# Kernel tuning notes

Measured on AMD Instinct MI355X. Metric: run time of the kernel, lower is better.

The kernel has to match this reference:

```python
import jax, jax.numpy as jnp
import numpy as np

H, W = 512, 512  # spatial shape from init_kwargs
N_PTS = 200000
C_IN, C_OUT, K, PAD = 64, 128, 3, 1


def setup_inputs() -> dict:
    key = jax.random.key(0)
    k1, k2, k3, k4 = jax.random.split(key, 4)
    batch_size = 4
    features = jax.random.normal(k1, (N_PTS, C_IN), dtype=jnp.float32)
    b = jax.random.randint(k2, (N_PTS, 1), 0, batch_size, dtype=jnp.int32)
    yx = jax.random.randint(k3, (N_PTS, 2), 0, H, dtype=jnp.int32)  # y,x in [0, 512)
    coors = jnp.concatenate([b, yx], axis=1)  # [N, 3] = (batch, y, x)
    # spconv conv weight, expressed OIHW for lax.conv
    weight = jax.random.normal(k4, (C_OUT, C_IN, K, K), dtype=jnp.float32) * (1.0 / np.sqrt(C_IN * K * K))
    return {"features": features, "coors": coors, "batch_size": batch_size, "weight": weight}


def reference(features, coors, batch_size, weight):
    # SparseConvTensor -> densify: scatter-add point features onto the [B, C, H, W] grid
    # (add is faithful to spconv's gather-GEMM-scatter handling of duplicate coords).
    dense = jnp.zeros((batch_size, features.shape[1], H, W), dtype=features.dtype)
    dense = dense.at[coors[:, 0], :, coors[:, 1], coors[:, 2]].add(features)
    # SparseConv2d(stride=1, padding=1, bias=None) == dense conv on the densified grid;
    # inactive output sites are exactly zero, so this matches the densified sparse output.
    out = jax.lax.conv_general_dilated(
        dense, weight,
        window_strides=(1, 1),
        padding=[(PAD, PAD), (PAD, PAD)],
        dimension_numbers=("NCHW", "OIHW", "NCHW"),
    )
    return out  # [B, C_out, H, W]
```

## Files before the change

kernel.cpp:

```cpp
#include <hip/hip_runtime.h>
#include <stdint.h>

#define HH 512
#define WW 512
#define CIN 64
#define COUT 128
#define NB 4
#define HP 514
#define WP 520
#define STRIP 128
#define SCOLS 136
#define NCHUNK 17
#define SLAB_B (SCOLS * CIN * 2)

typedef __bf16 bf16x8 __attribute__((ext_vector_type(8)));
typedef float f32x4 __attribute__((ext_vector_type(4)));
typedef const __attribute__((address_space(1))) uint32_t guint_t;
typedef __attribute__((address_space(3))) uint32_t luint_t;

__device__ __forceinline__ unsigned short f2bf(float f) {
    union { float f; uint32_t u; } v; v.f = f;
    uint32_t u = v.u;
    u += 0x7fffu + ((u >> 16) & 1u);
    return (unsigned short)(u >> 16);
}
__device__ __forceinline__ float bf2f(uint32_t u) {
    union { uint32_t u; float f; } v; v.u = u << 16;
    return v.f;
}

__global__ void zero_kernel(float4* __restrict__ p, long n4) {
    long i = (long)blockIdx.x * 256 + threadIdx.x;
    const long stride = (long)gridDim.x * 256;
    const float4 z = make_float4(0.f, 0.f, 0.f, 0.f);
    for (; i < n4; i += stride) p[i] = z;
}

__global__ void wt_transform(const float* __restrict__ w, unsigned short* __restrict__ wt2) {
    int tid = blockIdx.x * 256 + threadIdx.x;
    if (tid >= COUT * 576) return;
    int co = tid / 576;
    int k  = tid - co * 576;
    int off = k >> 6;
    int ci  = k & 63;
    int ky = off / 3;
    int kx = off - ky * 3;
    float val = w[((co * CIN + ci) * 3 + ky) * 3 + kx];
    wt2[(size_t)(k >> 3) * (COUT * 8) + co * 8 + (k & 7)] = f2bf(val);
}

__global__ void scatter_kernel(const float* __restrict__ feat,
                               const int* __restrict__ coors,
                               uint32_t* __restrict__ dpad, int npts) {
    int t = blockIdx.x * 256 + threadIdx.x;
    int p = t >> 5;
    int c2 = t & 31;
    if (p >= npts) return;
    int b = coors[p * 3 + 0];
    int y = coors[p * 3 + 1];
    int x = coors[p * 3 + 2];
    uint32_t* wp = dpad + (((size_t)b * HP + (y + 1)) * WP + (x + 1)) * (CIN / 2) + c2;
    float ax = feat[(size_t)p * CIN + c2 * 2];
    float ay = feat[(size_t)p * CIN + c2 * 2 + 1];
    uint32_t old = *wp, assumed;
    do {
        assumed = old;
        uint32_t nv = (uint32_t)f2bf(bf2f(assumed & 0xffffu) + ax)
                    | ((uint32_t)f2bf(bf2f(assumed >> 16) + ay) << 16);
        old = atomicCAS(wp, assumed, nv);
    } while (old != assumed);
}

__global__ __launch_bounds__(256, 3) void conv_kernel(
        const __bf16* __restrict__ dpad,
        const __bf16* __restrict__ wt2,
        float* __restrict__ out) {
    __shared__ __align__(16) __bf16 lds[3 * SCOLS * CIN];

    const int bid = blockIdx.x;
    const int xs = bid & 3;
    const int y  = (bid >> 2) & 511;
    const int b  = bid >> 11;
    const int x0 = xs * STRIP;
    const int tid = threadIdx.x;
    const int wave = tid >> 6;
    const int lane = tid & 63;
    const int lhi = lane >> 4;
    const int llo = lane & 15;
    const int site_base = (wave & 1) * 64;
    const int co_base   = (wave >> 1) * 64;

    const char* gbase = (const char*)dpad;
    #pragma unroll
    for (int r = 0; r < 3; ++r) {
        const char* rowp = gbase + (((size_t)b * HP + (y + r)) * WP + x0) * (CIN * 2);
        char* lslab = ((char*)lds) + r * SLAB_B;
        #pragma unroll
        for (int i = 0; i < 5; ++i) {
            int c = wave + i * 4;
            if (c < NCHUNK) {
                int P = c * 1024 + lane * 16;
                int L = P ^ (((P >> 7) & 7) << 4);
                __builtin_amdgcn_global_load_lds(
                    (guint_t*)(rowp + L), (luint_t*)(lslab + c * 1024), 16, 0, 0);
            }
        }
    }
    __syncthreads();

    f32x4 acc[4][4];
    #pragma unroll
    for (int mt = 0; mt < 4; ++mt)
        #pragma unroll
        for (int nt = 0; nt < 4; ++nt)
            acc[mt][nt] = (f32x4){0.f, 0.f, 0.f, 0.f};

    #pragma unroll
    for (int off = 0; off < 9; ++off) {
        const int ky = off / 3;
        const int kx = off - ky * 3;
        const char* slab = (const char*)lds + ky * SLAB_B;
        #pragma unroll
        for (int ch = 0; ch < 2; ++ch) {
            bf16x8 a[4];
            #pragma unroll
            for (int mt = 0; mt < 4; ++mt) {
                int col = site_base + mt * 16 + llo + kx;
                int eb = (ch * 64 + lhi * 16) ^ ((col & 7) << 4);
                a[mt] = *reinterpret_cast<const bf16x8*>(slab + col * 128 + eb);
            }
            const __bf16* bb = wt2 + (size_t)(off * 8 + ch * 4 + lhi) * (COUT * 8);
            #pragma unroll
            for (int nt = 0; nt < 4; ++nt) {
                bf16x8 bw = *reinterpret_cast<const bf16x8*>(
                    &bb[(co_base + nt * 16 + llo) * 8]);
                #pragma unroll
                for (int mt = 0; mt < 4; ++mt)
                    acc[mt][nt] = __builtin_amdgcn_mfma_f32_16x16x32_bf16(
                        a[mt], bw, acc[mt][nt], 0, 0, 0);
            }
        }
    }

    #pragma unroll
    for (int nt = 0; nt < 4; ++nt) {
        int co = co_base + nt * 16 + llo;
        float* orow = out + ((size_t)(b * COUT + co) * HH + y) * WW
                          + x0 + site_base + lhi * 4;
        #pragma unroll
        for (int mt = 0; mt < 4; ++mt)
            __builtin_nontemporal_store(acc[mt][nt],
                reinterpret_cast<f32x4*>(&orow[mt * 16]));
    }
}

extern "C" void kernel_launch(void* const* d_in, const int* in_sizes, int n_in,
                              void* d_out, int out_size, void* d_ws, size_t ws_size,
                              hipStream_t stream) {
    const float* feat  = (const float*)d_in[0];
    const int*   coors = (const int*)d_in[1];
    const float* w     = (const float*)d_in[3];
    float* out = (float*)d_out;

    const size_t dpad_bytes = (size_t)NB * HP * WP * CIN * 2;
    __bf16* dpad = (__bf16*)d_ws;
    unsigned short* wt2 = (unsigned short*)((char*)d_ws + dpad_bytes);

    const int npts = in_sizes[0] / CIN;

    hipLaunchKernelGGL(zero_kernel, dim3(2048), dim3(256), 0, stream,
                       (float4*)dpad, (long)(dpad_bytes / 16));
    hipLaunchKernelGGL(wt_transform, dim3((COUT * 576 + 255) / 256), dim3(256), 0, stream,
                       w, wt2);
    hipLaunchKernelGGL(scatter_kernel, dim3((npts * 32 + 255) / 256), dim3(256), 0, stream,
                       feat, coors, (uint32_t*)dpad, npts);
    hipLaunchKernelGGL(conv_kernel, dim3(NB * 512 * (WW / STRIP)), dim3(256), 0, stream,
                       dpad, (const __bf16*)wt2, out);
}
```

Before: 265.0 us.

## Compute two output rows per block with 32x32x16 MFMA tiles

Each conv block now loads four padded input rows into LDS and produces two output rows, so every loaded weight fragment is reused across both rows. The MFMA shape moves from 16x16x32 to 32x32x16, which raises arithmetic per operand fetch. The output store pattern is remapped to the 32x32 accumulator layout. In exchange, the grid has half as many blocks, LDS per block grows by a third, and the launch bound drops to 2 waves per SIMD, which lowers occupancy.

```diff
diff --git a/kernel.cpp b/kernel.cpp
--- a/kernel.cpp
+++ b/kernel.cpp
@@ -15,6 +15,7 @@
 
 typedef __bf16 bf16x8 __attribute__((ext_vector_type(8)));
 typedef float f32x4 __attribute__((ext_vector_type(4)));
+typedef float f32x16 __attribute__((ext_vector_type(16)));
 typedef const __attribute__((address_space(1))) uint32_t guint_t;
 typedef __attribute__((address_space(3))) uint32_t luint_t;
 
@@ -71,29 +72,30 @@
     } while (old != assumed);
 }
 
-__global__ __launch_bounds__(256, 3) void conv_kernel(
+__global__ __launch_bounds__(256, 2) void conv_kernel(
         const __bf16* __restrict__ dpad,
         const __bf16* __restrict__ wt2,
         float* __restrict__ out) {
-    __shared__ __align__(16) __bf16 lds[3 * SCOLS * CIN];
+    __shared__ __align__(16) __bf16 lds[4 * SCOLS * CIN];
 
     const int bid = blockIdx.x;
     const int xs = bid & 3;
-    const int y  = (bid >> 2) & 511;
-    const int b  = bid >> 11;
+    const int yb = (bid >> 2) & 255;
+    const int b  = bid >> 10;
     const int x0 = xs * STRIP;
+    const int y0 = yb * 2;
     const int tid = threadIdx.x;
     const int wave = tid >> 6;
     const int lane = tid & 63;
-    const int lhi = lane >> 4;
-    const int llo = lane & 15;
+    const int lo5 = lane & 31;
+    const int hi  = lane >> 5;
     const int site_base = (wave & 1) * 64;
     const int co_base   = (wave >> 1) * 64;
 
     const char* gbase = (const char*)dpad;
     #pragma unroll
-    for (int r = 0; r < 3; ++r) {
-        const char* rowp = gbase + (((size_t)b * HP + (y + r)) * WP + x0) * (CIN * 2);
+    for (int r = 0; r < 4; ++r) {
+        const char* rowp = gbase + (((size_t)b * HP + (y0 + r)) * WP + x0) * (CIN * 2);
         char* lslab = ((char*)lds) + r * SLAB_B;
         #pragma unroll
         for (int i = 0; i < 5; ++i) {
@@ -108,49 +110,67 @@
     }
     __syncthreads();
 
-    f32x4 acc[4][4];
+    f32x16 acc[2][2][2];
     #pragma unroll
-    for (int mt = 0; mt < 4; ++mt)
+    for (int r = 0; r < 2; ++r)
         #pragma unroll
-        for (int nt = 0; nt < 4; ++nt)
-            acc[mt][nt] = (f32x4){0.f, 0.f, 0.f, 0.f};
+        for (int mt = 0; mt < 2; ++mt)
+            #pragma unroll
+            for (int nt = 0; nt < 2; ++nt)
+                acc[r][mt][nt] = (f32x16){0.f,0.f,0.f,0.f,0.f,0.f,0.f,0.f,
+                                          0.f,0.f,0.f,0.f,0.f,0.f,0.f,0.f};
 
     #pragma unroll
     for (int off = 0; off < 9; ++off) {
         const int ky = off / 3;
         const int kx = off - ky * 3;
-        const char* slab = (const char*)lds + ky * SLAB_B;
         #pragma unroll
-        for (int ch = 0; ch < 2; ++ch) {
-            bf16x8 a[4];
+        for (int ch4 = 0; ch4 < 4; ++ch4) {
+            const __bf16* bb = wt2 + (size_t)(off * 8 + ch4 * 2 + hi) * (COUT * 8);
+            bf16x8 bw[2];
             #pragma unroll
-            for (int mt = 0; mt < 4; ++mt) {
-                int col = site_base + mt * 16 + llo + kx;
-                int eb = (ch * 64 + lhi * 16) ^ ((col & 7) << 4);
-                a[mt] = *reinterpret_cast<const bf16x8*>(slab + col * 128 + eb);
-            }
-            const __bf16* bb = wt2 + (size_t)(off * 8 + ch * 4 + lhi) * (COUT * 8);
+            for (int nt = 0; nt < 2; ++nt)
+                bw[nt] = *reinterpret_cast<const bf16x8*>(
+                    &bb[(co_base + nt * 32 + lo5) * 8]);
             #pragma unroll
-            for (int nt = 0; nt < 4; ++nt) {
-                bf16x8 bw = *reinterpret_cast<const bf16x8*>(
-                    &bb[(co_base + nt * 16 + llo) * 8]);
+            for (int r = 0; r < 2; ++r) {
+                const char* slab = (const char*)lds + (r + ky) * SLAB_B;
+                bf16x8 a[2];
                 #pragma unroll
-                for (int mt = 0; mt < 4; ++mt)
-                    acc[mt][nt] = __builtin_amdgcn_mfma_f32_16x16x32_bf16(
-                        a[mt], bw, acc[mt][nt], 0, 0, 0);
+                for (int mt = 0; mt < 2; ++mt) {
+                    int col = site_base + mt * 32 + lo5 + kx;
+                    int eb = (ch4 * 32 + hi * 16) ^ ((col & 7) << 4);
+                    a[mt] = *reinterpret_cast<const bf16x8*>(slab + col * 128 + eb);
+                }
+                #pragma unroll
+                for (int nt = 0; nt < 2; ++nt)
+                    #pragma unroll
+                    for (int mt = 0; mt < 2; ++mt)
+                        acc[r][mt][nt] = __builtin_amdgcn_mfma_f32_32x32x16_bf16(
+                            a[mt], bw[nt], acc[r][mt][nt], 0, 0, 0);
             }
         }
     }
 
     #pragma unroll
-    for (int nt = 0; nt < 4; ++nt) {
-        int co = co_base + nt * 16 + llo;
-        float* orow = out + ((size_t)(b * COUT + co) * HH + y) * WW
-                          + x0 + site_base + lhi * 4;
+    for (int r = 0; r < 2; ++r) {
+        const int y = y0 + r;
         #pragma unroll
-        for (int mt = 0; mt < 4; ++mt)
-            __builtin_nontemporal_store(acc[mt][nt],
-                reinterpret_cast<f32x4*>(&orow[mt * 16]));
+        for (int nt = 0; nt < 2; ++nt) {
+            const int co = co_base + nt * 32 + lo5;
+            float* orow = out + ((size_t)(b * COUT + co) * HH + y) * WW
+                              + x0 + site_base + hi * 4;
+            #pragma unroll
+            for (int mt = 0; mt < 2; ++mt) {
+                #pragma unroll
+                for (int q = 0; q < 4; ++q) {
+                    f32x4 v = { acc[r][mt][nt][q * 4 + 0], acc[r][mt][nt][q * 4 + 1],
+                                acc[r][mt][nt][q * 4 + 2], acc[r][mt][nt][q * 4 + 3] };
+                    __builtin_nontemporal_store(v,
+                        reinterpret_cast<f32x4*>(&orow[mt * 32 + q * 8]));
+                }
+            }
+        }
     }
 }
 
@@ -174,6 +194,6 @@
                        w, wt2);
     hipLaunchKernelGGL(scatter_kernel, dim3((npts * 32 + 255) / 256), dim3(256), 0, stream,
                        feat, coors, (uint32_t*)dpad, npts);
-    hipLaunchKernelGGL(conv_kernel, dim3(NB * 512 * (WW / STRIP)), dim3(256), 0, stream,
+    hipLaunchKernelGGL(conv_kernel, dim3(NB * 256 * (WW / STRIP)), dim3(256), 0, stream,
                        dpad, (const __bf16*)wt2, out);
 }
```

Result: slower. 411.7 us (+55.3%).

## Compute two output rows per conv block and fuse zero/weight-transform kernels

Applied to the files above, without the earlier changes.

The conv kernel now has each block compute two adjacent output rows. It stages four input rows in LDS instead of three, so the overlapping input rows and each weight fragment load are shared across both rows. The accumulator count doubles, and launch bounds drop from 3 to 2 blocks per CU to make room for the extra registers, which lowers occupancy. Separately, the zero-fill and weight-transform kernels are merged into one launch to save a kernel launch.

```diff
diff --git a/kernel.cpp b/kernel.cpp
--- a/kernel.cpp
+++ b/kernel.cpp
@@ -29,24 +29,24 @@
     return v.f;
 }
 
-__global__ void zero_kernel(float4* __restrict__ p, long n4) {
+__global__ void init_kernel(float4* __restrict__ dz, long n4,
+                            const float* __restrict__ w,
+                            unsigned short* __restrict__ wt2) {
     long i = (long)blockIdx.x * 256 + threadIdx.x;
     const long stride = (long)gridDim.x * 256;
     const float4 z = make_float4(0.f, 0.f, 0.f, 0.f);
-    for (; i < n4; i += stride) p[i] = z;
-}
-
-__global__ void wt_transform(const float* __restrict__ w, unsigned short* __restrict__ wt2) {
-    int tid = blockIdx.x * 256 + threadIdx.x;
-    if (tid >= COUT * 576) return;
-    int co = tid / 576;
-    int k  = tid - co * 576;
-    int off = k >> 6;
-    int ci  = k & 63;
-    int ky = off / 3;
-    int kx = off - ky * 3;
-    float val = w[((co * CIN + ci) * 3 + ky) * 3 + kx];
-    wt2[(size_t)(k >> 3) * (COUT * 8) + co * 8 + (k & 7)] = f2bf(val);
+    for (long j = i; j < n4; j += stride) dz[j] = z;
+    int tid = (int)i;
+    if (tid < COUT * 576) {
+        int co = tid / 576;
+        int k  = tid - co * 576;
+        int off = k >> 6;
+        int ci  = k & 63;
+        int ky = off / 3;
+        int kx = off - ky * 3;
+        float val = w[((co * CIN + ci) * 3 + ky) * 3 + kx];
+        wt2[(size_t)(k >> 3) * (COUT * 8) + co * 8 + (k & 7)] = f2bf(val);
+    }
 }
 
 __global__ void scatter_kernel(const float* __restrict__ feat,
@@ -71,17 +71,18 @@
     } while (old != assumed);
 }
 
-__global__ __launch_bounds__(256, 3) void conv_kernel(
+__global__ __launch_bounds__(256, 2) void conv_kernel(
         const __bf16* __restrict__ dpad,
         const __bf16* __restrict__ wt2,
         float* __restrict__ out) {
-    __shared__ __align__(16) __bf16 lds[3 * SCOLS * CIN];
+    __shared__ __align__(16) __bf16 lds[4 * SCOLS * CIN];
 
     const int bid = blockIdx.x;
     const int xs = bid & 3;
-    const int y  = (bid >> 2) & 511;
-    const int b  = bid >> 11;
+    const int yb = (bid >> 2) & 255;
+    const int b  = bid >> 10;
     const int x0 = xs * STRIP;
+    const int y0 = yb * 2;
     const int tid = threadIdx.x;
     const int wave = tid >> 6;
     const int lane = tid & 63;
@@ -92,8 +93,8 @@
 
     const char* gbase = (const char*)dpad;
     #pragma unroll
-    for (int r = 0; r < 3; ++r) {
-        const char* rowp = gbase + (((size_t)b * HP + (y + r)) * WP + x0) * (CIN * 2);
+    for (int r = 0; r < 4; ++r) {
+        const char* rowp = gbase + (((size_t)b * HP + (y0 + r)) * WP + x0) * (CIN * 2);
         char* lslab = ((char*)lds) + r * SLAB_B;
         #pragma unroll
         for (int i = 0; i < 5; ++i) {
@@ -108,49 +109,60 @@
     }
     __syncthreads();
 
-    f32x4 acc[4][4];
+    f32x4 acc[2][4][4];
     #pragma unroll
-    for (int mt = 0; mt < 4; ++mt)
+    for (int r = 0; r < 2; ++r)
         #pragma unroll
-        for (int nt = 0; nt < 4; ++nt)
-            acc[mt][nt] = (f32x4){0.f, 0.f, 0.f, 0.f};
+        for (int mt = 0; mt < 4; ++mt)
+            #pragma unroll
+            for (int nt = 0; nt < 4; ++nt)
+                acc[r][mt][nt] = (f32x4){0.f, 0.f, 0.f, 0.f};
 
     #pragma unroll
     for (int off = 0; off < 9; ++off) {
         const int ky = off / 3;
         const int kx = off - ky * 3;
-        const char* slab = (const char*)lds + ky * SLAB_B;
         #pragma unroll
         for (int ch = 0; ch < 2; ++ch) {
-            bf16x8 a[4];
+            const __bf16* bb = wt2 + (size_t)(off * 8 + ch * 4 + lhi) * (COUT * 8);
+            bf16x8 bw[4];
             #pragma unroll
-            for (int mt = 0; mt < 4; ++mt) {
-                int col = site_base + mt * 16 + llo + kx;
-                int eb = (ch * 64 + lhi * 16) ^ ((col & 7) << 4);
-                a[mt] = *reinterpret_cast<const bf16x8*>(slab + col * 128 + eb);
-            }
-            const __bf16* bb = wt2 + (size_t)(off * 8 + ch * 4 + lhi) * (COUT * 8);
+            for (int nt = 0; nt < 4; ++nt)
+                bw[nt] = *reinterpret_cast<const bf16x8*>(
+                    &bb[(co_base + nt * 16 + llo) * 8]);
             #pragma unroll
-            for (int nt = 0; nt < 4; ++nt) {
-                bf16x8 bw = *reinterpret_cast<const bf16x8*>(
-                    &bb[(co_base + nt * 16 + llo) * 8]);
+            for (int r = 0; r < 2; ++r) {
+                const char* slab = (const char*)lds + (r + ky) * SLAB_B;
+                bf16x8 a[4];
                 #pragma unroll
-                for (int mt = 0; mt < 4; ++mt)
-                    acc[mt][nt] = __builtin_amdgcn_mfma_f32_16x16x32_bf16(
-                        a[mt], bw, acc[mt][nt], 0, 0, 0);
+                for (int mt = 0; mt < 4; ++mt) {
+                    int col = site_base + mt * 16 + llo + kx;
+                    int eb = (ch * 64 + lhi * 16) ^ ((col & 7) << 4);
+                    a[mt] = *reinterpret_cast<const bf16x8*>(slab + col * 128 + eb);
+                }
+                #pragma unroll
+                for (int nt = 0; nt < 4; ++nt)
+                    #pragma unroll
+                    for (int mt = 0; mt < 4; ++mt)
+                        acc[r][mt][nt] = __builtin_amdgcn_mfma_f32_16x16x32_bf16(
+                            a[mt], bw[nt], acc[r][mt][nt], 0, 0, 0);
             }
         }
     }
 
     #pragma unroll
-    for (int nt = 0; nt < 4; ++nt) {
-        int co = co_base + nt * 16 + llo;
-        float* orow = out + ((size_t)(b * COUT + co) * HH + y) * WW
-                          + x0 + site_base + lhi * 4;
+    for (int r = 0; r < 2; ++r) {
+        const int y = y0 + r;
         #pragma unroll
-        for (int mt = 0; mt < 4; ++mt)
-            __builtin_nontemporal_store(acc[mt][nt],
-                reinterpret_cast<f32x4*>(&orow[mt * 16]));
+        for (int nt = 0; nt < 4; ++nt) {
+            int co = co_base + nt * 16 + llo;
+            float* orow = out + ((size_t)(b * COUT + co) * HH + y) * WW
+                              + x0 + site_base + lhi * 4;
+            #pragma unroll
+            for (int mt = 0; mt < 4; ++mt)
+                __builtin_nontemporal_store(acc[r][mt][nt],
+                    reinterpret_cast<f32x4*>(&orow[mt * 16]));
+        }
     }
 }
 
@@ -168,12 +180,10 @@
 
     const int npts = in_sizes[0] / CIN;
 
-    hipLaunchKernelGGL(zero_kernel, dim3(2048), dim3(256), 0, stream,
-                       (float4*)dpad, (long)(dpad_bytes / 16));
-    hipLaunchKernelGGL(wt_transform, dim3((COUT * 576 + 255) / 256), dim3(256), 0, stream,
-                       w, wt2);
+    hipLaunchKernelGGL(init_kernel, dim3(2048), dim3(256), 0, stream,
+                       (float4*)dpad, (long)(dpad_bytes / 16), w, wt2);
     hipLaunchKernelGGL(scatter_kernel, dim3((npts * 32 + 255) / 256), dim3(256), 0, stream,
                        feat, coors, (uint32_t*)dpad, npts);
-    hipLaunchKernelGGL(conv_kernel, dim3(NB * 512 * (WW / STRIP)), dim3(256), 0, stream,
+    hipLaunchKernelGGL(conv_kernel, dim3(NB * 256 * (WW / STRIP)), dim3(256), 0, stream,
                        dpad, (const __bf16*)wt2, out);
 }
```

After: 278.3 us. 1.05x slower.

## Replace dense scatter grid with binned point lists gathered directly into LDS

Applied to the files above, without the earlier changes.

Drops the zeroing of the padded dense bf16 grid and the atomic CAS scatter into it. Points are now counted and bucketed by (batch, row, 128-column strip) with a counting sort. The conv kernel then builds its three input rows in LDS by walking the point lists of neighbouring bins and accumulating features there. Weight transform is fused into the count kernel. This avoids the large dense write and read traffic, but adds a serial single-block scan, serial per-wave point loops inside the conv kernel, and order-dependent bf16 accumulation.

```diff
diff --git a/kernel.cpp b/kernel.cpp
--- a/kernel.cpp
+++ b/kernel.cpp
@@ -6,17 +6,14 @@
 #define CIN 64
 #define COUT 128
 #define NB 4
-#define HP 514
-#define WP 520
 #define STRIP 128
-#define SCOLS 136
-#define NCHUNK 17
+#define NXS (WW / STRIP)
+#define NBINS (NB * HH * NXS)
+#define SCOLS 130
 #define SLAB_B (SCOLS * CIN * 2)
 
 typedef __bf16 bf16x8 __attribute__((ext_vector_type(8)));
 typedef float f32x4 __attribute__((ext_vector_type(4)));
-typedef const __attribute__((address_space(1))) uint32_t guint_t;
-typedef __attribute__((address_space(3))) uint32_t luint_t;
 
 __device__ __forceinline__ unsigned short f2bf(float f) {
     union { float f; uint32_t u; } v; v.f = f;
@@ -29,50 +26,70 @@
     return v.f;
 }
 
-__global__ void zero_kernel(float4* __restrict__ p, long n4) {
-    long i = (long)blockIdx.x * 256 + threadIdx.x;
-    const long stride = (long)gridDim.x * 256;
-    const float4 z = make_float4(0.f, 0.f, 0.f, 0.f);
-    for (; i < n4; i += stride) p[i] = z;
-}
-
-__global__ void wt_transform(const float* __restrict__ w, unsigned short* __restrict__ wt2) {
-    int tid = blockIdx.x * 256 + threadIdx.x;
-    if (tid >= COUT * 576) return;
-    int co = tid / 576;
-    int k  = tid - co * 576;
-    int off = k >> 6;
-    int ci  = k & 63;
-    int ky = off / 3;
-    int kx = off - ky * 3;
-    float val = w[((co * CIN + ci) * 3 + ky) * 3 + kx];
-    wt2[(size_t)(k >> 3) * (COUT * 8) + co * 8 + (k & 7)] = f2bf(val);
-}
-
-__global__ void scatter_kernel(const float* __restrict__ feat,
-                               const int* __restrict__ coors,
-                               uint32_t* __restrict__ dpad, int npts) {
+__global__ void count_wt_kernel(const int* __restrict__ coors, int npts,
+                                int* __restrict__ cnt,
+                                const float* __restrict__ w,
+                                unsigned short* __restrict__ wt2) {
     int t = blockIdx.x * 256 + threadIdx.x;
-    int p = t >> 5;
-    int c2 = t & 31;
+    if (t < npts) {
+        int b = coors[t * 3 + 0];
+        int y = coors[t * 3 + 1];
+        int x = coors[t * 3 + 2];
+        atomicAdd(&cnt[((b << 9) + y) * NXS + (x >> 7)], 1);
+    }
+    if (t < COUT * 576) {
+        int co = t / 576;
+        int k  = t - co * 576;
+        int off = k >> 6;
+        int ci  = k & 63;
+        int ky = off / 3;
+        int kx = off - ky * 3;
+        float val = w[((co * CIN + ci) * 3 + ky) * 3 + kx];
+        wt2[(size_t)(k >> 3) * (COUT * 8) + co * 8 + (k & 7)] = f2bf(val);
+    }
+}
+
+__global__ void scan_kernel(const int* __restrict__ cnt,
+                            int* __restrict__ off, int* __restrict__ cur) {
+    __shared__ int part[256];
+    int t = threadIdx.x;
+    int base = t * 32;
+    int s = 0;
+    for (int i = 0; i < 32; ++i) s += cnt[base + i];
+    part[t] = s;
+    __syncthreads();
+    if (t == 0) {
+        int run = 0;
+        for (int i = 0; i < 256; ++i) { int v = part[i]; part[i] = run; run += v; }
+        off[NBINS] = run;
+    }
+    __syncthreads();
+    int run = part[t];
+    for (int i = 0; i < 32; ++i) {
+        int bin = base + i;
+        int v = cnt[bin];
+        off[bin] = run;
+        cur[bin] = run;
+        run += v;
+    }
+}
+
+__global__ void fill_kernel(const int* __restrict__ coors, int npts,
+                            int* __restrict__ cur, int* __restrict__ idx) {
+    int p = blockIdx.x * 256 + threadIdx.x;
     if (p >= npts) return;
     int b = coors[p * 3 + 0];
     int y = coors[p * 3 + 1];
     int x = coors[p * 3 + 2];
-    uint32_t* wp = dpad + (((size_t)b * HP + (y + 1)) * WP + (x + 1)) * (CIN / 2) + c2;
-    float ax = feat[(size_t)p * CIN + c2 * 2];
-    float ay = feat[(size_t)p * CIN + c2 * 2 + 1];
-    uint32_t old = *wp, assumed;
-    do {
-        assumed = old;
-        uint32_t nv = (uint32_t)f2bf(bf2f(assumed & 0xffffu) + ax)
-                    | ((uint32_t)f2bf(bf2f(assumed >> 16) + ay) << 16);
-        old = atomicCAS(wp, assumed, nv);
-    } while (old != assumed);
+    int bin = ((b << 9) + y) * NXS + (x >> 7);
+    int pos = atomicAdd(&cur[bin], 1);
+    idx[pos] = p | (x << 18);
 }
 
 __global__ __launch_bounds__(256, 3) void conv_kernel(
-        const __bf16* __restrict__ dpad,
+        const float* __restrict__ feat,
+        const int* __restrict__ off,
+        const int* __restrict__ idx,
         const __bf16* __restrict__ wt2,
         float* __restrict__ out) {
     __shared__ __align__(16) __bf16 lds[3 * SCOLS * CIN];
@@ -90,19 +107,41 @@
     const int site_base = (wave & 1) * 64;
     const int co_base   = (wave >> 1) * 64;
 
-    const char* gbase = (const char*)dpad;
-    #pragma unroll
-    for (int r = 0; r < 3; ++r) {
-        const char* rowp = gbase + (((size_t)b * HP + (y + r)) * WP + x0) * (CIN * 2);
-        char* lslab = ((char*)lds) + r * SLAB_B;
-        #pragma unroll
-        for (int i = 0; i < 5; ++i) {
-            int c = wave + i * 4;
-            if (c < NCHUNK) {
-                int P = c * 1024 + lane * 16;
-                int L = P ^ (((P >> 7) & 7) << 4);
-                __builtin_amdgcn_global_load_lds(
-                    (guint_t*)(rowp + L), (luint_t*)(lslab + c * 1024), 16, 0, 0);
+    {
+        const int n16 = 3 * SLAB_B / 16;
+        f32x4* l4 = reinterpret_cast<f32x4*>(lds);
+        for (int i = tid; i < n16; i += 256)
+            l4[i] = (f32x4){0.f, 0.f, 0.f, 0.f};
+    }
+    __syncthreads();
+
+    const int irow = y - 1 + wave;
+    if (wave < 3 && (unsigned)irow < HH) {
+        char* slab = (char*)lds + wave * SLAB_B;
+        const int binrow = ((b << 9) + irow) * NXS;
+        #pragma unroll
+        for (int nb = -1; nb <= 1; ++nb) {
+            int xsn = xs + nb;
+            if ((unsigned)xsn < NXS) {
+                int s = off[binrow + xsn];
+                int e = off[binrow + xsn + 1];
+                for (int j = s; j < e; ++j) {
+                    int v = idx[j];
+                    int xp = v >> 18;
+                    int col = xp + 1 - x0;
+                    if ((unsigned)col <= 129u && lane < 32) {
+                        int p = v & 0x3ffff;
+                        int o = lane << 2;
+                        uint32_t* slot = (uint32_t*)(slab + col * 128
+                                                     + (o ^ ((col & 7) << 4)));
+                        float fx = feat[(size_t)p * CIN + lane * 2];
+                        float fy = feat[(size_t)p * CIN + lane * 2 + 1];
+                        uint32_t c = *slot;
+                        uint32_t nx = f2bf(bf2f(c & 0xffffu) + fx);
+                        uint32_t ny = f2bf(bf2f(c >> 16) + fy);
+                        *slot = nx | (ny << 16);
+                    }
+                }
             }
         }
     }
@@ -116,9 +155,9 @@
             acc[mt][nt] = (f32x4){0.f, 0.f, 0.f, 0.f};
 
     #pragma unroll
-    for (int off = 0; off < 9; ++off) {
-        const int ky = off / 3;
-        const int kx = off - ky * 3;
+    for (int off9 = 0; off9 < 9; ++off9) {
+        const int ky = off9 / 3;
+        const int kx = off9 - ky * 3;
         const char* slab = (const char*)lds + ky * SLAB_B;
         #pragma unroll
         for (int ch = 0; ch < 2; ++ch) {
@@ -129,7 +168,7 @@
                 int eb = (ch * 64 + lhi * 16) ^ ((col & 7) << 4);
                 a[mt] = *reinterpret_cast<const bf16x8*>(slab + col * 128 + eb);
             }
-            const __bf16* bb = wt2 + (size_t)(off * 8 + ch * 4 + lhi) * (COUT * 8);
+            const __bf16* bb = wt2 + (size_t)(off9 * 8 + ch * 4 + lhi) * (COUT * 8);
             #pragma unroll
             for (int nt = 0; nt < 4; ++nt) {
                 bf16x8 bw = *reinterpret_cast<const bf16x8*>(
@@ -162,18 +201,25 @@
     const float* w     = (const float*)d_in[3];
     float* out = (float*)d_out;
 
-    const size_t dpad_bytes = (size_t)NB * HP * WP * CIN * 2;
-    __bf16* dpad = (__bf16*)d_ws;
-    unsigned short* wt2 = (unsigned short*)((char*)d_ws + dpad_bytes);
-
     const int npts = in_sizes[0] / CIN;
 
-    hipLaunchKernelGGL(zero_kernel, dim3(2048), dim3(256), 0, stream,
-                       (float4*)dpad, (long)(dpad_bytes / 16));
-    hipLaunchKernelGGL(wt_transform, dim3((COUT * 576 + 255) / 256), dim3(256), 0, stream,
-                       w, wt2);
-    hipLaunchKernelGGL(scatter_kernel, dim3((npts * 32 + 255) / 256), dim3(256), 0, stream,
-                       feat, coors, (uint32_t*)dpad, npts);
-    hipLaunchKernelGGL(conv_kernel, dim3(NB * 512 * (WW / STRIP)), dim3(256), 0, stream,
-                       dpad, (const __bf16*)wt2, out);
-}
+    int* cnt = (int*)d_ws;
+    int* off = cnt + NBINS;
+    int* cur = off + NBINS + 1;
+    int* idx = cur + NBINS;
+    uintptr_t wa = (uintptr_t)(idx + npts);
+    wa = (wa + 15) & ~(uintptr_t)15;
+    unsigned short* wt2 = (unsigned short*)wa;
+
+    hipMemsetAsync(cnt, 0, NBINS * sizeof(int), stream);
+
+    int cw_grid = (npts > COUT * 576 ? npts : COUT * 576);
+    hipLaunchKernelGGL(count_wt_kernel, dim3((cw_grid + 255) / 256), dim3(256), 0, stream,
+                       coors, npts, cnt, w, wt2);
+    hipLaunchKernelGGL(scan_kernel, dim3(1), dim3(256), 0, stream,
+                       cnt, off, cur);
+    hipLaunchKernelGGL(fill_kernel, dim3((npts + 255) / 256), dim3(256), 0, stream,
+                       coors, npts, cur, idx);
+    hipLaunchKernelGGL(conv_kernel, dim3(NB * HH * NXS), dim3(256), 0, stream,
+                       feat, off, idx, (const __bf16*)wt2, out);
+}
```

Result: slower. 457.5 us (+72.6%).
